# Kernel tuning notes

Measured on AMD Instinct MI355X. Metric: run time of the kernel, lower is better.

Reference implementation:

```python
import jax, jax.numpy as jnp
import numpy as np

SCALE_FACTORS = (0.5, 1.0)
ITERATIONS = (2, 2)
TAU = (1.0, 1.0)
SIGMA = (1.0, 1.0)
SIGMA_CUTOFF = 3.0
EPS = 1e-9
DHW = ('NCDHW', 'OIDHW', 'NCDHW')


def gaussian_kernel1d(sigma):
    radius = int(round(sigma * SIGMA_CUTOFF))
    x = np.arange(-radius, radius + 1, dtype=np.float32)
    k = np.exp(-0.5 * (x / sigma) ** 2)
    return jnp.asarray(k / k.sum())


def smooth3d(vf, kernel):
    # separable depthwise Gaussian over the 3 spatial axes; vf: (B,C,D,H,W)
    C = vf.shape[1]
    n = kernel.shape[0]
    for axis in range(3):
        shape = [1, 1, 1]
        shape[axis] = n
        kern = jnp.broadcast_to(kernel.reshape(1, 1, *shape), (C, 1, *shape))
        vf = jax.lax.conv_general_dilated(vf, kern, (1, 1, 1), 'SAME',
                                          feature_group_count=C, dimension_numbers=DHW)
    return vf


def resize_tri(x, spatial):
    return jax.image.resize(x, x.shape[:2] + tuple(spatial), method='trilinear')


def warp(img, flow):
    # trilinear grid-sample with voxel-space displacement, border clamping
    B, C, D, H, W = img.shape
    gz, gy, gx = jnp.meshgrid(jnp.arange(D, dtype=img.dtype),
                              jnp.arange(H, dtype=img.dtype),
                              jnp.arange(W, dtype=img.dtype), indexing='ij')
    base = jnp.stack([gz, gy, gx])  # (3,D,H,W)

    def one(im, fl):
        z = jnp.clip(base[0] + fl[0], 0.0, D - 1)
        y = jnp.clip(base[1] + fl[1], 0.0, H - 1)
        x = jnp.clip(base[2] + fl[2], 0.0, W - 1)
        z0 = jnp.floor(z); y0 = jnp.floor(y); x0 = jnp.floor(x)
        wz = z - z0; wy = y - y0; wx = x - x0
        z0i = z0.astype(jnp.int32); y0i = y0.astype(jnp.int32); x0i = x0.astype(jnp.int32)
        z1i = jnp.minimum(z0i + 1, D - 1)
        y1i = jnp.minimum(y0i + 1, H - 1)
        x1i = jnp.minimum(x0i + 1, W - 1)

        def g(zi, yi, xi):
            return im[:, zi, yi, xi]  # (C,D,H,W)

        return (g(z0i, y0i, x0i) * (1 - wz) * (1 - wy) * (1 - wx)
                + g(z0i, y0i, x1i) * (1 - wz) * (1 - wy) * wx
                + g(z0i, y1i, x0i) * (1 - wz) * wy * (1 - wx)
                + g(z0i, y1i, x1i) * (1 - wz) * wy * wx
                + g(z1i, y0i, x0i) * wz * (1 - wy) * (1 - wx)
                + g(z1i, y0i, x1i) * wz * (1 - wy) * wx
                + g(z1i, y1i, x0i) * wz * wy * (1 - wx)
                + g(z1i, y1i, x1i) * wz * wy * wx)

    return jax.vmap(one)(img, flow)


def demon_forces(warped, fixed):
    # 'active' demon forces: gradient of the warped moving image
    diff = warped - fixed                                  # (B,1,D,H,W)
    g = jnp.stack(jnp.gradient(warped[:, 0], axis=(1, 2, 3)), axis=1)  # (B,3,D,H,W)
    denom = jnp.sum(g * g, axis=1, keepdims=True) + diff * diff + EPS
    return diff * g / denom


def conv3(x, w, b=None):
    y = jax.lax.conv_general_dilated(x, w, (1, 1, 1), 'SAME', dimension_numbers=DHW)
    return y if b is None else y + b.reshape(1, -1, 1, 1, 1)


def inorm(x):  # InstanceNorm3d, affine=False, eps=1e-5
    m = x.mean(axis=(2, 3, 4), keepdims=True)
    v = x.var(axis=(2, 3, 4), keepdims=True)
    return (x - m) * jax.lax.rsqrt(v + 1e-5)


def mish(x):
    return x * jnp.tanh(jax.nn.softplus(x))


def updater(x, w1, w2, w3, w4, b4):
    x = mish(inorm(conv3(x, w1)))
    x = mish(inorm(conv3(x, w2)))
    x = mish(inorm(conv3(x, w3)))
    return conv3(x, w4, b4)


def match_vf(vf, spatial):
    old = vf.shape[2:]
    if tuple(old) == tuple(spatial):
        return vf
    vf2 = resize_tri(vf, spatial)
    scale = jnp.array([s1 / s2 for s1, s2 in zip(spatial, old)], dtype=vf.dtype)
    return vf2 * scale.reshape(1, 3, 1, 1, 1)


def registration(image, moving, w1, w2, w3, w4, b4):
    vf = None
    for i, (sf, iters) in enumerate(zip(SCALE_FACTORS, ITERATIONS)):
        spatial = tuple(int(s * sf) for s in image.shape[2:])
        si = resize_tri(image, spatial)
        smov = resize_tri(moving, spatial)
        vf = jnp.zeros((image.shape[0], 3) + spatial, image.dtype) if vf is None else match_vf(vf, spatial)
        kernel = gaussian_kernel1d(SIGMA[i]).astype(image.dtype)
        for _ in range(iters):
            warped = warp(smov, vf)
            forces = demon_forces(warped, si)
            feat = jnp.concatenate([forces, si, warped], axis=1)  # 5 channels
            vf = vf + TAU[i] * updater(feat, w1, w2, w3, w4, b4)
            vf = smooth3d(vf, kernel)
    vf = match_vf(vf, image.shape[2:])
    warped_full = warp(moving, vf)
    return warped_full, vf


def setup_inputs() -> dict:
    key = jax.random.key(0)
    ks = jax.random.split(key, 8)
    D = H = W = 96
    return {
        'image': jax.random.uniform(ks[0], (1, 1, D, H, W), jnp.float32),
        'mask': jnp.ones((1, 1, D, H, W), jnp.float32),
        'moving': jax.random.uniform(ks[1], (1, 1, D, H, W), jnp.float32),
        'spacing': jnp.ones((3,), jnp.float32),
        'w1': jax.random.normal(ks[2], (32, 5, 3, 3, 3), jnp.float32) * 0.05,
        'w2': jax.random.normal(ks[3], (64, 32, 3, 3, 3), jnp.float32) * 0.05,
        'w3': jax.random.normal(ks[4], (32, 64, 3, 3, 3), jnp.float32) * 0.05,
        'w4': jax.random.normal(ks[5], (3, 32, 3, 3, 3), jnp.float32) * 0.05,
        'b4': jnp.zeros((3,), jnp.float32),
    }


def reference(image, mask, moving, spacing, w1, w2, w3, w4, b4):
    # mask only feeds metrics/early-stopping (disabled: early_stopping_fn='none');
    # spacing unused since use_image_spacing=False.
    return registration(image, moving, w1, w2, w3, w4, b4)
```

## Files before the change

kernel.cpp:

```cpp
#include <hip/hip_runtime.h>
#include <hip/hip_bf16.h>


#define DEV __device__ __forceinline__
typedef __hip_bfloat16 bf16;
typedef __attribute__((ext_vector_type(8))) short short8;
typedef __attribute__((ext_vector_type(4))) float f32x4;

DEV float bfu(unsigned int u) {
  union { unsigned int i; float f; } x; x.i = u << 16; return x.f;
}
DEV unsigned short fbf(float f) {
  __hip_bfloat16 h = __float2bfloat16(f);
  return __builtin_bit_cast(unsigned short, h);
}

__global__ void zero_k(float* __restrict__ p, int n) {
  int i = blockIdx.x * 256 + threadIdx.x;
  if (i < n) p[i] = 0.f;
}
__global__ void copy_k(const float* __restrict__ in, float* __restrict__ out, int n) {
  int i = blockIdx.x * 256 + threadIdx.x;
  if (i < n) out[i] = in[i];
}

__global__ void pack_wf_k(const float* __restrict__ w, bf16* __restrict__ dst,
                          int NWT, int KB, int COR, int CIR) {
  int idx = blockIdx.x * 256 + threadIdx.x;
  int tot = 27 * NWT * KB * 512;
  if (idx >= tot) return;
  int j = idx & 7;
  int lane = (idx >> 3) & 63;
  int frag = idx >> 9;
  int kb = frag % KB;
  int r2 = frag / KB;
  int nwt = r2 % NWT;
  int off = r2 / NWT;
  int lid = lane & 15, kg = lane >> 4;
  int co = nwt * 16 + lid;
  int ci = (kb * 4 + kg) * 8 + j;
  float v = (co < COR && ci < CIR) ? w[((size_t)co * CIR + ci) * 27 + off] : 0.f;
  dst[idx] = __float2bfloat16(v);
}

DEV int ds_taps(int i, int n_out, int* j0, float* w) {
  if (i == 0) { *j0 = 0; w[0] = 3.f/7.f; w[1] = 3.f/7.f; w[2] = 1.f/7.f; return 3; }
  if (i == n_out - 1) { *j0 = 2*i - 1; w[0] = 1.f/7.f; w[1] = 3.f/7.f; w[2] = 3.f/7.f; return 3; }
  *j0 = 2*i - 1; w[0] = 0.125f; w[1] = 0.375f; w[2] = 0.375f; w[3] = 0.125f; return 4;
}
DEV void up_taps(int i, int n_in, int* j0, int* j1, float* w0, float* w1) {
  if (i & 1) {
    int k = i >> 1;
    if (k + 1 >= n_in) { *j0 = n_in - 1; *j1 = n_in - 1; *w0 = 1.f; *w1 = 0.f; }
    else { *j0 = k; *j1 = k + 1; *w0 = 0.75f; *w1 = 0.25f; }
  } else {
    int k = i >> 1;
    if (k == 0) { *j0 = 0; *j1 = 0; *w0 = 1.f; *w1 = 0.f; }
    else { *j0 = k - 1; *j1 = k; *w0 = 0.25f; *w1 = 0.75f; }
  }
}

__global__ void down2x_k(const float* __restrict__ in, float* __restrict__ out,
                         int Do, int Ho, int Wo) {
  const int Hi = 2 * Ho, Wi = 2 * Wo;
  const int No = Do * Ho * Wo;
  int i = blockIdx.x * 256 + threadIdx.x;
  if (i >= No) return;
  int xo = i % Wo; int t = i / Wo; int yo = t % Ho; int zo = t / Ho;
  int jz0, jy0, jx0; float wz[4], wy[4], wx[4];
  int cz = ds_taps(zo, Do, &jz0, wz);
  int cy = ds_taps(yo, Ho, &jy0, wy);
  int cx = ds_taps(xo, Wo, &jx0, wx);
  float s = 0.f;
  for (int a = 0; a < cz; ++a) {
    const float* pz = in + (size_t)(jz0 + a) * Hi * Wi;
    for (int b = 0; b < cy; ++b) {
      const float* py = pz + (size_t)(jy0 + b) * Wi;
      float wab = wz[a] * wy[b];
      for (int d = 0; d < cx; ++d) s += wab * wx[d] * py[jx0 + d];
    }
  }
  out[i] = s;
}

__global__ void up2x_vf_k(const float* __restrict__ in, float* __restrict__ out,
                          int Do, int Ho, int Wo) {
  const int Di = Do / 2, Hi = Ho / 2, Wi = Wo / 2;
  const int No = Do * Ho * Wo;
  const int c = blockIdx.y;
  int i = blockIdx.x * 256 + threadIdx.x;
  if (i >= No) return;
  int xo = i % Wo; int t = i / Wo; int yo = t % Ho; int zo = t / Ho;
  int jz0, jz1, jy0, jy1, jx0, jx1; float wz0, wz1, wy0, wy1, wx0, wx1;
  up_taps(zo, Di, &jz0, &jz1, &wz0, &wz1);
  up_taps(yo, Hi, &jy0, &jy1, &wy0, &wy1);
  up_taps(xo, Wi, &jx0, &jx1, &wx0, &wx1);
  const float* p = in + (size_t)c * Di * Hi * Wi;
  float v00 = wx0 * p[(jz0 * Hi + jy0) * Wi + jx0] + wx1 * p[(jz0 * Hi + jy0) * Wi + jx1];
  float v01 = wx0 * p[(jz0 * Hi + jy1) * Wi + jx0] + wx1 * p[(jz0 * Hi + jy1) * Wi + jx1];
  float v10 = wx0 * p[(jz1 * Hi + jy0) * Wi + jx0] + wx1 * p[(jz1 * Hi + jy0) * Wi + jx1];
  float v11 = wx0 * p[(jz1 * Hi + jy1) * Wi + jx0] + wx1 * p[(jz1 * Hi + jy1) * Wi + jx1];
  float s = wz0 * (wy0 * v00 + wy1 * v01) + wz1 * (wy0 * v10 + wy1 * v11);
  out[(size_t)c * No + i] = 2.f * s;
}

__global__ void warp_k(const float* __restrict__ img, const float* __restrict__ vf,
                       float* __restrict__ out, int D, int H, int W) {
  const int N = D * H * W;
  int i = blockIdx.x * 256 + threadIdx.x;
  if (i >= N) return;
  int x = i % W; int t = i / W; int y = t % H; int z = t / H;
  float zc = fminf(fmaxf((float)z + vf[i], 0.f), (float)(D - 1));
  float yc = fminf(fmaxf((float)y + vf[(size_t)N + i], 0.f), (float)(H - 1));
  float xc = fminf(fmaxf((float)x + vf[2 * (size_t)N + i], 0.f), (float)(W - 1));
  float zf = floorf(zc), yf = floorf(yc), xf = floorf(xc);
  int z0 = (int)zf, y0 = (int)yf, x0 = (int)xf;
  float wz = zc - zf, wy = yc - yf, wx = xc - xf;
  int z1 = min(z0 + 1, D - 1), y1 = min(y0 + 1, H - 1), x1 = min(x0 + 1, W - 1);
  const int HW = H * W;
  float v000 = img[z0 * HW + y0 * W + x0];
  float v001 = img[z0 * HW + y0 * W + x1];
  float v010 = img[z0 * HW + y1 * W + x0];
  float v011 = img[z0 * HW + y1 * W + x1];
  float v100 = img[z1 * HW + y0 * W + x0];
  float v101 = img[z1 * HW + y0 * W + x1];
  float v110 = img[z1 * HW + y1 * W + x0];
  float v111 = img[z1 * HW + y1 * W + x1];
  float r = v000 * (1 - wz) * (1 - wy) * (1 - wx)
          + v001 * (1 - wz) * (1 - wy) * wx
          + v010 * (1 - wz) * wy * (1 - wx)
          + v011 * (1 - wz) * wy * wx
          + v100 * wz * (1 - wy) * (1 - wx)
          + v101 * wz * (1 - wy) * wx
          + v110 * wz * wy * (1 - wx)
          + v111 * wz * wy * wx;
  out[i] = r;
}

__global__ void forces8_k(const float* __restrict__ wpd, const float* __restrict__ si,
                          bf16* __restrict__ feat, int D, int H, int W) {
  const int N = D * H * W;
  int i = blockIdx.x * 256 + threadIdx.x;
  if (i >= N) return;
  int x = i % W; int t = i / W; int y = t % H; int z = t / H;
  float wv = wpd[i];
  const int HW = H * W;
  float gz = (z == 0) ? (wpd[i + HW] - wv) : (z == D - 1) ? (wv - wpd[i - HW]) : 0.5f * (wpd[i + HW] - wpd[i - HW]);
  float gy = (y == 0) ? (wpd[i + W] - wv) : (y == H - 1) ? (wv - wpd[i - W]) : 0.5f * (wpd[i + W] - wpd[i - W]);
  float gx = (x == 0) ? (wpd[i + 1] - wv) : (x == W - 1) ? (wv - wpd[i - 1]) : 0.5f * (wpd[i + 1] - wpd[i - 1]);
  float s = si[i];
  float diff = wv - s;
  float denom = gz * gz + gy * gy + gx * gx + diff * diff + 1e-9f;
  short8 o;
  o[0] = (short)fbf((diff * gz) / denom);
  o[1] = (short)fbf((diff * gy) / denom);
  o[2] = (short)fbf((diff * gx) / denom);
  o[3] = (short)fbf(s);
  o[4] = (short)fbf(wv);
  o[5] = 0; o[6] = 0; o[7] = 0;
  *(short8*)((short*)feat + (size_t)i * 8) = o;
}

template <int CIN, int COUT, int TZ, int TY, int INS, int REDUCE>
__global__ void __launch_bounds__(512) convmf_k(
    const bf16* __restrict__ act, const bf16* __restrict__ wpk,
    bf16* __restrict__ out, double* __restrict__ pbuf, int D, int H, int W) {
  constexpr int CH = CIN / 8;
  constexpr int HZ = TZ + 2, HY = TY + 2;
  constexpr int HALO = HZ * HY * 18;
  constexpr int MS = TZ * TY / 4;
  constexpr int NS = COUT / 32;
  constexpr int NWT = COUT / 16;
  constexpr int KB = CIN / 32;
  __shared__ short lds[HALO * CIN];
  __shared__ float2 red[8][NS][16];
  const int t = threadIdx.x;
  const int gx0 = blockIdx.x * 16, gy0 = blockIdx.y * TY, gz0 = blockIdx.z * TZ;
  const short* actS = (const short*)act;
  for (int cid = t; cid < HALO * CH; cid += 512) {
    int pos = cid / CH, c = cid - pos * CH;
    int hx = pos % 18; int r = pos / 18; int hy = r % HY; int hz = r / HY;
    int gz = gz0 + hz - 1, gy = gy0 + hy - 1, gx = gx0 + hx - 1;
    uint4 v = {0u, 0u, 0u, 0u};
    if (((unsigned)gz < (unsigned)D) & ((unsigned)gy < (unsigned)H) & ((unsigned)gx < (unsigned)W)) {
      size_t vox = (size_t)(gz * H + gy) * W + gx;
      if (INS == 8) { if (c == 0) v = *(const uint4*)(actS + vox * 8); }
      else v = *(const uint4*)(actS + vox * CIN + c * 8);
    }
    *(uint4*)(lds + pos * CIN + ((c ^ (pos & (CH - 1))) * 8)) = v;
  }
  __syncthreads();
  const int lane = t & 63, wid = t >> 6;
  const int mw = wid & 3, nw = wid >> 2;
  const int lid = lane & 15, kg = lane >> 4;
  f32x4 acc[MS][NS];
#pragma unroll
  for (int ms = 0; ms < MS; ++ms)
#pragma unroll
    for (int n = 0; n < NS; ++n) acc[ms][n] = {0.f, 0.f, 0.f, 0.f};
  int rowpos[MS];
#pragma unroll
  for (int ms = 0; ms < MS; ++ms) {
    int r = mw * MS + ms;
    rowpos[ms] = ((r / TY) * HY + (r % TY)) * 18 + lid;
  }
  const short* wp = (const short*)wpk;
#pragma unroll 1
  for (int kz = 0; kz < 3; ++kz)
#pragma unroll 1
    for (int ky = 0; ky < 3; ++ky) {
      const int delta0 = (kz * HY + ky) * 18;
#pragma unroll
      for (int kx = 0; kx < 3; ++kx) {
        const int off = (kz * 3 + ky) * 3 + kx;
        short8 bq[NS][KB];
#pragma unroll
        for (int n = 0; n < NS; ++n)
#pragma unroll
          for (int kb = 0; kb < KB; ++kb)
            bq[n][kb] = *(const short8*)(wp + ((((size_t)off * NWT + nw * NS + n) * KB + kb) << 9) + lane * 8);
#pragma unroll
        for (int ms = 0; ms < MS; ++ms) {
          int pos = rowpos[ms] + delta0 + kx;
          int sw = pos & (CH - 1);
#pragma unroll
          for (int kb = 0; kb < KB; ++kb) {
            short8 a = *(const short8*)(lds + pos * CIN + (((kb * 4 + kg) ^ sw) * 8));
#pragma unroll
            for (int n = 0; n < NS; ++n)
              acc[ms][n] = __builtin_amdgcn_mfma_f32_16x16x32_bf16(a, bq[n][kb], acc[ms][n], 0, 0, 0);
          }
        }
      }
    }
  const int xe = kg * 4;
#pragma unroll
  for (int ms = 0; ms < MS; ++ms) {
    int r = mw * MS + ms;
    int z = gz0 + r / TY, y = gy0 + r % TY;
    size_t voxb = (size_t)(z * H + y) * W + gx0;
#pragma unroll
    for (int n = 0; n < NS; ++n) {
      int co = nw * NS * 16 + n * 16 + lid;
#pragma unroll
      for (int rg = 0; rg < 4; ++rg)
        out[(voxb + xe + rg) * COUT + co] = __float2bfloat16(acc[ms][n][rg]);
    }
  }
  if (REDUCE) {
#pragma unroll
    for (int n = 0; n < NS; ++n) {
      float s = 0.f, q = 0.f;
#pragma unroll
      for (int ms = 0; ms < MS; ++ms)
#pragma unroll
        for (int rg = 0; rg < 4; ++rg) {
          float v = acc[ms][n][rg];
          s += v; q += v * v;
        }
      s += __shfl_xor(s, 16); q += __shfl_xor(q, 16);
      s += __shfl_xor(s, 32); q += __shfl_xor(q, 32);
      if (lane < 16) red[wid][n][lane] = make_float2(s, q);
    }
    __syncthreads();
    if (t < COUT) {
      const int nw_ = t / (NS * 16);
      const int rem = t - nw_ * NS * 16;
      const int n_ = rem >> 4, lid_ = rem & 15;
      float S = 0.f, Q = 0.f;
#pragma unroll
      for (int m = 0; m < 4; ++m) {
        float2 v = red[nw_ * 4 + m][n_][lid_];
        S += v.x; Q += v.y;
      }
      const int G = gridDim.x * gridDim.y * gridDim.z;
      const int bid = blockIdx.x + gridDim.x * (blockIdx.y + gridDim.y * blockIdx.z);
      pbuf[((size_t)t * G + bid) * 2 + 0] = (double)S;
      pbuf[((size_t)t * G + bid) * 2 + 1] = (double)Q;
    }
  }
}

template <int TZ, int TY>
__global__ void __launch_bounds__(512) conv4mf_k(
    const bf16* __restrict__ act, const bf16* __restrict__ wpk,
    const float* __restrict__ bias, float* __restrict__ vf, int D, int H, int W) {
  constexpr int CH = 4;
  constexpr int HZ = TZ + 2, HY = TY + 2;
  constexpr int HALO = HZ * HY * 18;
  constexpr int MS = TZ * TY / 8;
  __shared__ short lds[HALO * 32];
  const int t = threadIdx.x;
  const int gx0 = blockIdx.x * 16, gy0 = blockIdx.y * TY, gz0 = blockIdx.z * TZ;
  const int N = D * H * W;
  const short* actS = (const short*)act;
  for (int cid = t; cid < HALO * CH; cid += 512) {
    int pos = cid / CH, c = cid - pos * CH;
    int hx = pos % 18; int r = pos / 18; int hy = r % HY; int hz = r / HY;
    int gz = gz0 + hz - 1, gy = gy0 + hy - 1, gx = gx0 + hx - 1;
    uint4 v = {0u, 0u, 0u, 0u};
    if (((unsigned)gz < (unsigned)D) & ((unsigned)gy < (unsigned)H) & ((unsigned)gx < (unsigned)W))
      v = *(const uint4*)(actS + ((size_t)(gz * H + gy) * W + gx) * 32 + c * 8);
    *(uint4*)(lds + pos * 32 + ((c ^ (pos & 3)) * 8)) = v;
  }
  __syncthreads();
  const int lane = t & 63, wid = t >> 6;
  const int lid = lane & 15, kg = lane >> 4;
  f32x4 acc[MS];
#pragma unroll
  for (int ms = 0; ms < MS; ++ms) acc[ms] = {0.f, 0.f, 0.f, 0.f};
  int rowpos[MS];
#pragma unroll
  for (int ms = 0; ms < MS; ++ms) {
    int r = wid * MS + ms;
    rowpos[ms] = ((r / TY) * HY + (r % TY)) * 18 + lid;
  }
  const short* wp = (const short*)wpk;
#pragma unroll 1
  for (int kz = 0; kz < 3; ++kz)
#pragma unroll 1
    for (int ky = 0; ky < 3; ++ky) {
      const int delta0 = (kz * HY + ky) * 18;
#pragma unroll
      for (int kx = 0; kx < 3; ++kx) {
        const int off = (kz * 3 + ky) * 3 + kx;
        short8 b = *(const short8*)(wp + ((size_t)off << 9) + lane * 8);
#pragma unroll
        for (int ms = 0; ms < MS; ++ms) {
          int pos = rowpos[ms] + delta0 + kx;
          int sw = pos & 3;
          short8 a = *(const short8*)(lds + pos * 32 + ((kg ^ sw) * 8));
          acc[ms] = __builtin_amdgcn_mfma_f32_16x16x32_bf16(a, b, acc[ms], 0, 0, 0);
        }
      }
    }
  if (lid < 3) {
    float bs = bias[lid];
#pragma unroll
    for (int ms = 0; ms < MS; ++ms) {
      int r = wid * MS + ms;
      int z = gz0 + r / TY, y = gy0 + r % TY;
      size_t voxb = (size_t)(z * H + y) * W + gx0 + kg * 4;
      float* p = vf + (size_t)lid * N + voxb;
#pragma unroll
      for (int rg = 0; rg < 4; ++rg) p[rg] += acc[ms][rg] + bs;
    }
  }
}

__global__ void stage2_k(const double* __restrict__ pbuf, float2* __restrict__ musc,
                         int N, int G) {
  const int c = blockIdx.x;
  double S = 0, Q = 0;
  for (int g = threadIdx.x; g < G; g += 256) {
    S += pbuf[((size_t)c * G + g) * 2 + 0];
    Q += pbuf[((size_t)c * G + g) * 2 + 1];
  }
  for (int off = 32; off > 0; off >>= 1) {
    S += __shfl_down(S, off); Q += __shfl_down(Q, off);
  }
  __shared__ double ls[4], lq[4];
  const int wid = threadIdx.x >> 6, lane = threadIdx.x & 63;
  if (lane == 0) { ls[wid] = S; lq[wid] = Q; }
  __syncthreads();
  if (threadIdx.x == 0) {
    double St = ls[0] + ls[1] + ls[2] + ls[3];
    double Qt = lq[0] + lq[1] + lq[2] + lq[3];
    double m = St / N;
    double var = Qt / N - m * m;
    musc[c] = make_float2((float)m, (float)(1.0 / sqrt(var + 1e-5)));
  }
}

DEV float mishf(float v) {
  if (v > 20.f) return v;
  float u = __expf(v);
  float w = u * (u + 2.f);
  return v * (w / (w + 2.f));
}

template <int C>
__global__ void inorm_vc_k(bf16* __restrict__ x, const float2* __restrict__ musc, int N) {
  constexpr int CP = C / 2;
  constexpr int VPB = 256 / CP;
  const int cp = threadIdx.x & (CP - 1);
  const int vt = threadIdx.x / CP;
  float2 m0 = musc[2 * cp], m1 = musc[2 * cp + 1];
  unsigned int* p = (unsigned int*)x;
  int v0 = blockIdx.x * (4 * VPB) + vt;
#pragma unroll
  for (int r = 0; r < 4; ++r) {
    int v = v0 + r * VPB;
    size_t idx = (size_t)v * CP + cp;
    unsigned int u = p[idx];
    float a = mishf((bfu(u & 0xffffu) - m0.x) * m0.y);
    float b = mishf((bfu(u >> 16) - m1.x) * m1.y);
    p[idx] = (unsigned int)fbf(a) | ((unsigned int)fbf(b) << 16);
  }
}

template <int AXIS>
__global__ void smooth_k(const float* __restrict__ in, float* __restrict__ out,
                         int D, int H, int W) {
  const int N = D * H * W;
  const int c = blockIdx.y;
  int i = blockIdx.x * 256 + threadIdx.x;
  if (i >= N) return;
  int x = i % W; int t = i / W; int y = t % H; int z = t / H;
  const int coord = AXIS == 0 ? z : AXIS == 1 ? y : x;
  const int len = AXIS == 0 ? D : AXIS == 1 ? H : W;
  const int stride = AXIS == 0 ? H * W : AXIS == 1 ? W : 1;
  const float k1 = 0.60653065971263342f, k2 = 0.13533528323661270f, k3 = 0.011108996538242306f;
  const float kn = 1.f / (1.f + 2.f * (k1 + k2 + k3));
  const float gw[4] = {kn, k1 * kn, k2 * kn, k3 * kn};
  const float* p = in + (size_t)c * N;
  float s = gw[0] * p[i];
#pragma unroll
  for (int tt = 1; tt <= 3; ++tt) {
    if (coord - tt >= 0) s += gw[tt] * p[i - tt * stride];
    if (coord + tt < len) s += gw[tt] * p[i + tt * stride];
  }
  out[(size_t)c * N + i] = s;
}

extern "C" void kernel_launch(void* const* d_in, const int* in_sizes, int n_in,
                              void* d_out, int out_size, void* d_ws, size_t ws_size,
                              hipStream_t stream) {
  const float* image  = (const float*)d_in[0];
  const float* moving = (const float*)d_in[2];
  const float* w1 = (const float*)d_in[4];
  const float* w2 = (const float*)d_in[5];
  const float* w3 = (const float*)d_in[6];
  const float* w4 = (const float*)d_in[7];
  const float* b4 = (const float*)d_in[8];
  float* out = (float*)d_out;

  const int D1 = 96; const int N1 = D1 * D1 * D1;
  const int D0 = 48; const int N0 = D0 * D0 * D0;

  char* wsp = (char*)d_ws;
  double* pbuf  = (double*)wsp;          wsp += (size_t)64 * 13824 * 2 * 8;
  float2* musc  = (float2*)wsp;          wsp += 1024;
  bf16* w1p     = (bf16*)wsp;            wsp += 27 * 2 * 1 * 512 * 2;
  bf16* w2p     = (bf16*)wsp;            wsp += 27 * 4 * 1 * 512 * 2;
  bf16* w3p     = (bf16*)wsp;            wsp += 27 * 2 * 2 * 512 * 2;
  bf16* w4p     = (bf16*)wsp;            wsp += 27 * 1 * 1 * 512 * 2;
  float* si0    = (float*)wsp;           wsp += (size_t)N0 * 4;
  float* smov0  = (float*)wsp;           wsp += (size_t)N0 * 4;
  float* vf0    = (float*)wsp;           wsp += 3 * (size_t)N1 * 4;
  float* vf1    = (float*)wsp;           wsp += 3 * (size_t)N1 * 4;
  float* warped = (float*)wsp;           wsp += (size_t)N1 * 4;
  bf16* feat    = (bf16*)wsp;            wsp += 8 * (size_t)N1 * 2;
  bf16* bufA    = (bf16*)wsp;            wsp += 32 * (size_t)N1 * 2;
  bf16* bufB    = (bf16*)wsp;            wsp += 64 * (size_t)N1 * 2;

  pack_wf_k<<<(27 * 2 * 512 + 255) / 256, 256, 0, stream>>>(w1, w1p, 2, 1, 32, 5);
  pack_wf_k<<<(27 * 4 * 512 + 255) / 256, 256, 0, stream>>>(w2, w2p, 4, 1, 64, 32);
  pack_wf_k<<<(27 * 4 * 512 + 255) / 256, 256, 0, stream>>>(w3, w3p, 2, 2, 32, 64);
  pack_wf_k<<<(27 * 1 * 512 + 255) / 256, 256, 0, stream>>>(w4, w4p, 1, 1, 3, 32);

  down2x_k<<<N0 / 256, 256, 0, stream>>>(image, si0, D0, D0, D0);
  down2x_k<<<N0 / 256, 256, 0, stream>>>(moving, smov0, D0, D0, D0);
  zero_k<<<3 * N0 / 256, 256, 0, stream>>>(vf0, 3 * N0);

  float* vfc = vf0;
  float* vfa = vf1;

  auto run_level = [&](const float* si, const float* smov, int Dd) {
    const int N = Dd * Dd * Dd;
    const int nb = N / 256;
    const dim3 g1(Dd / 16, Dd / 4, Dd / 4);
    const dim3 g3(Dd / 16, Dd / 4, Dd / 2);
    const int G1 = g1.x * g1.y * g1.z;
    const int G3 = g3.x * g3.y * g3.z;
    for (int it = 0; it < 2; ++it) {
      warp_k<<<nb, 256, 0, stream>>>(smov, vfc, warped, Dd, Dd, Dd);
      forces8_k<<<nb, 256, 0, stream>>>(warped, si, feat, Dd, Dd, Dd);

      convmf_k<32, 32, 4, 4, 8, 1><<<g1, 512, 0, stream>>>(feat, w1p, bufA, pbuf, Dd, Dd, Dd);
      stage2_k<<<32, 256, 0, stream>>>(pbuf, musc, N, G1);
      inorm_vc_k<32><<<N / 64, 256, 0, stream>>>(bufA, musc, N);

      convmf_k<32, 64, 4, 4, 32, 1><<<g1, 512, 0, stream>>>(bufA, w2p, bufB, pbuf, Dd, Dd, Dd);
      stage2_k<<<64, 256, 0, stream>>>(pbuf, musc, N, G1);
      inorm_vc_k<64><<<N / 32, 256, 0, stream>>>(bufB, musc, N);

      convmf_k<64, 32, 2, 4, 64, 1><<<g3, 512, 0, stream>>>(bufB, w3p, bufA, pbuf, Dd, Dd, Dd);
      stage2_k<<<32, 256, 0, stream>>>(pbuf, musc, N, G3);
      inorm_vc_k<32><<<N / 64, 256, 0, stream>>>(bufA, musc, N);

      conv4mf_k<4, 4><<<g1, 512, 0, stream>>>(bufA, w4p, b4, vfc, Dd, Dd, Dd);

      smooth_k<0><<<dim3(nb, 3), 256, 0, stream>>>(vfc, vfa, Dd, Dd, Dd);
      smooth_k<1><<<dim3(nb, 3), 256, 0, stream>>>(vfa, vfc, Dd, Dd, Dd);
      smooth_k<2><<<dim3(nb, 3), 256, 0, stream>>>(vfc, vfa, Dd, Dd, Dd);
      { float* tmp = vfc; vfc = vfa; vfa = tmp; }
    }
  };

  run_level(si0, smov0, D0);

  up2x_vf_k<<<dim3(N1 / 256, 3), 256, 0, stream>>>(vfc, vfa, D1, D1, D1);
  { float* tmp = vfc; vfc = vfa; vfa = tmp; }

  run_level(image, moving, D1);

  warp_k<<<N1 / 256, 256, 0, stream>>>(moving, vfc, out, D1, D1, D1);
  copy_k<<<3 * N1 / 256, 256, 0, stream>>>(vfc, out + N1, 3 * N1);
}
```

Baseline: 1.353 ms.

## Use smaller 2x4 spatial tiles with one row per wave in MFMA convs

```diff
diff --git a/kernel.cpp b/kernel.cpp
--- a/kernel.cpp
+++ b/kernel.cpp
@@ -161,16 +161,15 @@
   *(short8*)((short*)feat + (size_t)i * 8) = o;
 }
 
-template <int CIN, int COUT, int TZ, int TY, int INS, int REDUCE>
+template <int CIN, int COUT, int INS, int REDUCE>
 __global__ void __launch_bounds__(512) convmf_k(
     const bf16* __restrict__ act, const bf16* __restrict__ wpk,
     bf16* __restrict__ out, double* __restrict__ pbuf, int D, int H, int W) {
+  constexpr int TZ = 2, TY = 4;
   constexpr int CH = CIN / 8;
   constexpr int HZ = TZ + 2, HY = TY + 2;
   constexpr int HALO = HZ * HY * 18;
-  constexpr int MS = TZ * TY / 4;
-  constexpr int NS = COUT / 32;
-  constexpr int NWT = COUT / 16;
+  constexpr int NS = COUT / 16;
   constexpr int KB = CIN / 32;
   __shared__ short lds[HALO * CIN];
   __shared__ float2 red[8][NS][16];
@@ -191,19 +190,11 @@
   }
   __syncthreads();
   const int lane = t & 63, wid = t >> 6;
-  const int mw = wid & 3, nw = wid >> 2;
   const int lid = lane & 15, kg = lane >> 4;
-  f32x4 acc[MS][NS];
-#pragma unroll
-  for (int ms = 0; ms < MS; ++ms)
-#pragma unroll
-    for (int n = 0; n < NS; ++n) acc[ms][n] = {0.f, 0.f, 0.f, 0.f};
-  int rowpos[MS];
-#pragma unroll
-  for (int ms = 0; ms < MS; ++ms) {
-    int r = mw * MS + ms;
-    rowpos[ms] = ((r / TY) * HY + (r % TY)) * 18 + lid;
-  }
+  f32x4 acc[NS];
+#pragma unroll
+  for (int n = 0; n < NS; ++n) acc[n] = {0.f, 0.f, 0.f, 0.f};
+  const int rowpos = ((wid / TY) * HY + (wid % TY)) * 18 + lid;
   const short* wp = (const short*)wpk;
 #pragma unroll 1
   for (int kz = 0; kz < 3; ++kz)
@@ -218,33 +209,28 @@
         for (int n = 0; n < NS; ++n)
 #pragma unroll
           for (int kb = 0; kb < KB; ++kb)
-            bq[n][kb] = *(const short8*)(wp + ((((size_t)off * NWT + nw * NS + n) * KB + kb) << 9) + lane * 8);
-#pragma unroll
-        for (int ms = 0; ms < MS; ++ms) {
-          int pos = rowpos[ms] + delta0 + kx;
-          int sw = pos & (CH - 1);
-#pragma unroll
-          for (int kb = 0; kb < KB; ++kb) {
-            short8 a = *(const short8*)(lds + pos * CIN + (((kb * 4 + kg) ^ sw) * 8));
-#pragma unroll
-            for (int n = 0; n < NS; ++n)
-              acc[ms][n] = __builtin_amdgcn_mfma_f32_16x16x32_bf16(a, bq[n][kb], acc[ms][n], 0, 0, 0);
-          }
+            bq[n][kb] = *(const short8*)(wp + ((((size_t)off * NS + n) * KB + kb) << 9) + lane * 8);
+        const int pos = rowpos + delta0 + kx;
+        const int sw = pos & (CH - 1);
+#pragma unroll
+        for (int kb = 0; kb < KB; ++kb) {
+          short8 a = *(const short8*)(lds + pos * CIN + (((kb * 4 + kg) ^ sw) * 8));
+#pragma unroll
+          for (int n = 0; n < NS; ++n)
+            acc[n] = __builtin_amdgcn_mfma_f32_16x16x32_bf16(a, bq[n][kb], acc[n], 0, 0, 0);
         }
       }
     }
   const int xe = kg * 4;
-#pragma unroll
-  for (int ms = 0; ms < MS; ++ms) {
-    int r = mw * MS + ms;
-    int z = gz0 + r / TY, y = gy0 + r % TY;
+  {
+    int z = gz0 + wid / TY, y = gy0 + wid % TY;
     size_t voxb = (size_t)(z * H + y) * W + gx0;
 #pragma unroll
     for (int n = 0; n < NS; ++n) {
-      int co = nw * NS * 16 + n * 16 + lid;
+      int co = n * 16 + lid;
 #pragma unroll
       for (int rg = 0; rg < 4; ++rg)
-        out[(voxb + xe + rg) * COUT + co] = __float2bfloat16(acc[ms][n][rg]);
+        out[(voxb + xe + rg) * COUT + co] = __float2bfloat16(acc[n][rg]);
     }
   }
   if (REDUCE) {
@@ -252,25 +238,21 @@
     for (int n = 0; n < NS; ++n) {
       float s = 0.f, q = 0.f;
 #pragma unroll
-      for (int ms = 0; ms < MS; ++ms)
-#pragma unroll
-        for (int rg = 0; rg < 4; ++rg) {
-          float v = acc[ms][n][rg];
-          s += v; q += v * v;
-        }
+      for (int rg = 0; rg < 4; ++rg) {
+        float v = acc[n][rg];
+        s += v; q += v * v;
+      }
       s += __shfl_xor(s, 16); q += __shfl_xor(q, 16);
       s += __shfl_xor(s, 32); q += __shfl_xor(q, 32);
       if (lane < 16) red[wid][n][lane] = make_float2(s, q);
     }
     __syncthreads();
     if (t < COUT) {
-      const int nw_ = t / (NS * 16);
-      const int rem = t - nw_ * NS * 16;
-      const int n_ = rem >> 4, lid_ = rem & 15;
+      const int n_ = t >> 4, lid_ = t & 15;
       float S = 0.f, Q = 0.f;
 #pragma unroll
-      for (int m = 0; m < 4; ++m) {
-        float2 v = red[nw_ * 4 + m][n_][lid_];
+      for (int m = 0; m < 8; ++m) {
+        float2 v = red[m][n_][lid_];
         S += v.x; Q += v.y;
       }
       const int G = gridDim.x * gridDim.y * gridDim.z;
@@ -281,14 +263,13 @@
   }
 }
 
-template <int TZ, int TY>
 __global__ void __launch_bounds__(512) conv4mf_k(
     const bf16* __restrict__ act, const bf16* __restrict__ wpk,
     const float* __restrict__ bias, float* __restrict__ vf, int D, int H, int W) {
+  constexpr int TZ = 2, TY = 4;
   constexpr int CH = 4;
   constexpr int HZ = TZ + 2, HY = TY + 2;
   constexpr int HALO = HZ * HY * 18;
-  constexpr int MS = TZ * TY / 8;
   __shared__ short lds[HALO * 32];
   const int t = threadIdx.x;
   const int gx0 = blockIdx.x * 16, gy0 = blockIdx.y * TY, gz0 = blockIdx.z * TZ;
@@ -306,15 +287,8 @@
   __syncthreads();
   const int lane = t & 63, wid = t >> 6;
   const int lid = lane & 15, kg = lane >> 4;
-  f32x4 acc[MS];
-#pragma unroll
-  for (int ms = 0; ms < MS; ++ms) acc[ms] = {0.f, 0.f, 0.f, 0.f};
-  int rowpos[MS];
-#pragma unroll
-  for (int ms = 0; ms < MS; ++ms) {
-    int r = wid * MS + ms;
-    rowpos[ms] = ((r / TY) * HY + (r % TY)) * 18 + lid;
-  }
+  f32x4 acc = {0.f, 0.f, 0.f, 0.f};
+  const int rowpos = ((wid / TY) * HY + (wid % TY)) * 18 + lid;
   const short* wp = (const short*)wpk;
 #pragma unroll 1
   for (int kz = 0; kz < 3; ++kz)
@@ -325,26 +299,19 @@
       for (int kx = 0; kx < 3; ++kx) {
         const int off = (kz * 3 + ky) * 3 + kx;
         short8 b = *(const short8*)(wp + ((size_t)off << 9) + lane * 8);
-#pragma unroll
-        for (int ms = 0; ms < MS; ++ms) {
-          int pos = rowpos[ms] + delta0 + kx;
-          int sw = pos & 3;
-          short8 a = *(const short8*)(lds + pos * 32 + ((kg ^ sw) * 8));
-          acc[ms] = __builtin_amdgcn_mfma_f32_16x16x32_bf16(a, b, acc[ms], 0, 0, 0);
-        }
+        const int pos = rowpos + delta0 + kx;
+        const int sw = pos & 3;
+        short8 a = *(const short8*)(lds + pos * 32 + ((kg ^ sw) * 8));
+        acc = __builtin_amdgcn_mfma_f32_16x16x32_bf16(a, b, acc, 0, 0, 0);
       }
     }
   if (lid < 3) {
     float bs = bias[lid];
-#pragma unroll
-    for (int ms = 0; ms < MS; ++ms) {
-      int r = wid * MS + ms;
-      int z = gz0 + r / TY, y = gy0 + r % TY;
-      size_t voxb = (size_t)(z * H + y) * W + gx0 + kg * 4;
-      float* p = vf + (size_t)lid * N + voxb;
-#pragma unroll
-      for (int rg = 0; rg < 4; ++rg) p[rg] += acc[ms][rg] + bs;
-    }
+    int z = gz0 + wid / TY, y = gy0 + wid % TY;
+    size_t voxb = (size_t)(z * H + y) * W + gx0 + kg * 4;
+    float* p = vf + (size_t)lid * N + voxb;
+#pragma unroll
+    for (int rg = 0; rg < 4; ++rg) p[rg] += acc[rg] + bs;
   }
 }
 
@@ -469,27 +436,25 @@
   auto run_level = [&](const float* si, const float* smov, int Dd) {
     const int N = Dd * Dd * Dd;
     const int nb = N / 256;
-    const dim3 g1(Dd / 16, Dd / 4, Dd / 4);
-    const dim3 g3(Dd / 16, Dd / 4, Dd / 2);
-    const int G1 = g1.x * g1.y * g1.z;
-    const int G3 = g3.x * g3.y * g3.z;
+    const dim3 gc(Dd / 16, Dd / 4, Dd / 2);
+    const int G = gc.x * gc.y * gc.z;
     for (int it = 0; it < 2; ++it) {
       warp_k<<<nb, 256, 0, stream>>>(smov, vfc, warped, Dd, Dd, Dd);
       forces8_k<<<nb, 256, 0, stream>>>(warped, si, feat, Dd, Dd, Dd);
 
-      convmf_k<32, 32, 4, 4, 8, 1><<<g1, 512, 0, stream>>>(feat, w1p, bufA, pbuf, Dd, Dd, Dd);
-      stage2_k<<<32, 256, 0, stream>>>(pbuf, musc, N, G1);
+      convmf_k<32, 32, 8, 1><<<gc, 512, 0, stream>>>(feat, w1p, bufA, pbuf, Dd, Dd, Dd);
+      stage2_k<<<32, 256, 0, stream>>>(pbuf, musc, N, G);
       inorm_vc_k<32><<<N / 64, 256, 0, stream>>>(bufA, musc, N);
 
-      convmf_k<32, 64, 4, 4, 32, 1><<<g1, 512, 0, stream>>>(bufA, w2p, bufB, pbuf, Dd, Dd, Dd);
-      stage2_k<<<64, 256, 0, stream>>>(pbuf, musc, N, G1);
+      convmf_k<32, 64, 32, 1><<<gc, 512, 0, stream>>>(bufA, w2p, bufB, pbuf, Dd, Dd, Dd);
+      stage2_k<<<64, 256, 0, stream>>>(pbuf, musc, N, G);
       inorm_vc_k<64><<<N / 32, 256, 0, stream>>>(bufB, musc, N);
 
-      convmf_k<64, 32, 2, 4, 64, 1><<<g3, 512, 0, stream>>>(bufB, w3p, bufA, pbuf, Dd, Dd, Dd);
-      stage2_k<<<32, 256, 0, stream>>>(pbuf, musc, N, G3);
+      convmf_k<64, 32, 64, 1><<<gc, 512, 0, stream>>>(bufB, w3p, bufA, pbuf, Dd, Dd, Dd);
+      stage2_k<<<32, 256, 0, stream>>>(pbuf, musc, N, G);
       inorm_vc_k<32><<<N / 64, 256, 0, stream>>>(bufA, musc, N);
 
-      conv4mf_k<4, 4><<<g1, 512, 0, stream>>>(bufA, w4p, b4, vfc, Dd, Dd, Dd);
+      conv4mf_k<<<gc, 512, 0, stream>>>(bufA, w4p, b4, vfc, Dd, Dd, Dd);
 
       smooth_k<0><<<dim3(nb, 3), 256, 0, stream>>>(vfc, vfa, Dd, Dd, Dd);
       smooth_k<1><<<dim3(nb, 3), 256, 0, stream>>>(vfa, vfc, Dd, Dd, Dd);
```

Result: slower. 1.813 ms (+34.0%).

## Switch conv kernels to 32x32x16 MFMA tiles and shrink conv1 channel padding

Applied to the files above, without the earlier changes.

```diff
diff --git a/kernel.cpp b/kernel.cpp
--- a/kernel.cpp
+++ b/kernel.cpp
@@ -6,6 +6,7 @@
 typedef __hip_bfloat16 bf16;
 typedef __attribute__((ext_vector_type(8))) short short8;
 typedef __attribute__((ext_vector_type(4))) float f32x4;
+typedef __attribute__((ext_vector_type(16))) float f32x16;
 
 DEV float bfu(unsigned int u) {
   union { unsigned int i; float f; } x; x.i = u << 16; return x.f;
@@ -36,9 +37,26 @@
   int r2 = frag / KB;
   int nwt = r2 % NWT;
   int off = r2 / NWT;
-  int lid = lane & 15, kg = lane >> 4;
-  int co = nwt * 16 + lid;
-  int ci = (kb * 4 + kg) * 8 + j;
+  int co = nwt * 16 + (lane & 15);
+  int ci = (kb * 4 + (lane >> 4)) * 8 + j;
+  float v = (co < COR && ci < CIR) ? w[((size_t)co * CIR + ci) * 27 + off] : 0.f;
+  dst[idx] = __float2bfloat16(v);
+}
+
+__global__ void pack_w32_k(const float* __restrict__ w, bf16* __restrict__ dst,
+                           int NT, int KB, int COR, int CIR) {
+  int idx = blockIdx.x * 256 + threadIdx.x;
+  int tot = 27 * NT * KB * 512;
+  if (idx >= tot) return;
+  int j = idx & 7;
+  int lane = (idx >> 3) & 63;
+  int frag = idx >> 9;
+  int kb = frag % KB;
+  int r2 = frag / KB;
+  int n = r2 % NT;
+  int off = r2 / NT;
+  int co = n * 32 + (lane & 31);
+  int ci = kb * 16 + (lane >> 5) * 8 + j;
   float v = (co < COR && ci < CIR) ? w[((size_t)co * CIR + ci) * 27 + off] : 0.f;
   dst[idx] = __float2bfloat16(v);
 }
@@ -161,23 +179,23 @@
   *(short8*)((short*)feat + (size_t)i * 8) = o;
 }
 
-template <int CIN, int COUT, int TZ, int TY, int INS, int REDUCE>
-__global__ void __launch_bounds__(512) convmf_k(
+template <int CIN, int COUT, int INS, int REDUCE, int TZ, int TY>
+__global__ void __launch_bounds__(TZ* TY * 32) convmf32_k(
     const bf16* __restrict__ act, const bf16* __restrict__ wpk,
     bf16* __restrict__ out, double* __restrict__ pbuf, int D, int H, int W) {
+  constexpr int WAVES = TZ * TY / 2;
+  constexpr int THREADS = WAVES * 64;
   constexpr int CH = CIN / 8;
   constexpr int HZ = TZ + 2, HY = TY + 2;
   constexpr int HALO = HZ * HY * 18;
-  constexpr int MS = TZ * TY / 4;
-  constexpr int NS = COUT / 32;
-  constexpr int NWT = COUT / 16;
-  constexpr int KB = CIN / 32;
+  constexpr int NT = COUT / 32;
+  constexpr int KB = CIN / 16;
   __shared__ short lds[HALO * CIN];
-  __shared__ float2 red[8][NS][16];
+  __shared__ float2 red[WAVES][NT][32];
   const int t = threadIdx.x;
   const int gx0 = blockIdx.x * 16, gy0 = blockIdx.y * TY, gz0 = blockIdx.z * TZ;
   const short* actS = (const short*)act;
-  for (int cid = t; cid < HALO * CH; cid += 512) {
+  for (int cid = t; cid < HALO * CH; cid += THREADS) {
     int pos = cid / CH, c = cid - pos * CH;
     int hx = pos % 18; int r = pos / 18; int hy = r % HY; int hz = r / HY;
     int gz = gz0 + hz - 1, gy = gy0 + hy - 1, gx = gx0 + hx - 1;
@@ -191,19 +209,15 @@
   }
   __syncthreads();
   const int lane = t & 63, wid = t >> 6;
-  const int mw = wid & 3, nw = wid >> 2;
-  const int lid = lane & 15, kg = lane >> 4;
-  f32x4 acc[MS][NS];
-#pragma unroll
-  for (int ms = 0; ms < MS; ++ms)
-#pragma unroll
-    for (int n = 0; n < NS; ++n) acc[ms][n] = {0.f, 0.f, 0.f, 0.f};
-  int rowpos[MS];
-#pragma unroll
-  for (int ms = 0; ms < MS; ++ms) {
-    int r = mw * MS + ms;
-    rowpos[ms] = ((r / TY) * HY + (r % TY)) * 18 + lid;
-  }
+  const int m = lane & 31;
+  const int g2 = lane >> 5;
+  f32x16 acc[NT];
+#pragma unroll
+  for (int n = 0; n < NT; ++n)
+#pragma unroll
+    for (int r16 = 0; r16 < 16; ++r16) acc[n][r16] = 0.f;
+  const int r = 2 * wid + (m >> 4);
+  const int rowpos = ((r / TY) * HY + (r % TY)) * 18 + (m & 15);
   const short* wp = (const short*)wpk;
 #pragma unroll 1
   for (int kz = 0; kz < 3; ++kz)
@@ -213,64 +227,52 @@
 #pragma unroll
       for (int kx = 0; kx < 3; ++kx) {
         const int off = (kz * 3 + ky) * 3 + kx;
-        short8 bq[NS][KB];
-#pragma unroll
-        for (int n = 0; n < NS; ++n)
+        short8 bq[NT][KB];
+#pragma unroll
+        for (int n = 0; n < NT; ++n)
 #pragma unroll
           for (int kb = 0; kb < KB; ++kb)
-            bq[n][kb] = *(const short8*)(wp + ((((size_t)off * NWT + nw * NS + n) * KB + kb) << 9) + lane * 8);
-#pragma unroll
-        for (int ms = 0; ms < MS; ++ms) {
-          int pos = rowpos[ms] + delta0 + kx;
-          int sw = pos & (CH - 1);
-#pragma unroll
-          for (int kb = 0; kb < KB; ++kb) {
-            short8 a = *(const short8*)(lds + pos * CIN + (((kb * 4 + kg) ^ sw) * 8));
-#pragma unroll
-            for (int n = 0; n < NS; ++n)
-              acc[ms][n] = __builtin_amdgcn_mfma_f32_16x16x32_bf16(a, bq[n][kb], acc[ms][n], 0, 0, 0);
-          }
+            bq[n][kb] = *(const short8*)(wp + ((((size_t)off * NT + n) * KB + kb) << 9) + lane * 8);
+        const int pos = rowpos + delta0 + kx;
+        const int sw = pos & (CH - 1);
+#pragma unroll
+        for (int kb = 0; kb < KB; ++kb) {
+          short8 a = *(const short8*)(lds + pos * CIN + (((kb * 2 + g2) ^ sw) * 8));
+#pragma unroll
+          for (int n = 0; n < NT; ++n)
+            acc[n] = __builtin_amdgcn_mfma_f32_32x32x16_bf16(a, bq[n][kb], acc[n], 0, 0, 0);
         }
       }
     }
-  const int xe = kg * 4;
-#pragma unroll
-  for (int ms = 0; ms < MS; ++ms) {
-    int r = mw * MS + ms;
-    int z = gz0 + r / TY, y = gy0 + r % TY;
-    size_t voxb = (size_t)(z * H + y) * W + gx0;
-#pragma unroll
-    for (int n = 0; n < NS; ++n) {
-      int co = nw * NS * 16 + n * 16 + lid;
-#pragma unroll
-      for (int rg = 0; rg < 4; ++rg)
-        out[(voxb + xe + rg) * COUT + co] = __float2bfloat16(acc[ms][n][rg]);
-    }
+#pragma unroll
+  for (int reg = 0; reg < 16; ++reg) {
+    const int mm = (reg & 3) + 8 * (reg >> 2) + 4 * g2;
+    const int rr = 2 * wid + (mm >> 4);
+    const int z = gz0 + rr / TY, y = gy0 + rr % TY;
+    const size_t vox = (size_t)(z * H + y) * W + gx0 + (mm & 15);
+#pragma unroll
+    for (int n = 0; n < NT; ++n)
+      out[vox * COUT + n * 32 + (lane & 31)] = __float2bfloat16(acc[n][reg]);
   }
   if (REDUCE) {
 #pragma unroll
-    for (int n = 0; n < NS; ++n) {
+    for (int n = 0; n < NT; ++n) {
       float s = 0.f, q = 0.f;
 #pragma unroll
-      for (int ms = 0; ms < MS; ++ms)
-#pragma unroll
-        for (int rg = 0; rg < 4; ++rg) {
-          float v = acc[ms][n][rg];
-          s += v; q += v * v;
-        }
-      s += __shfl_xor(s, 16); q += __shfl_xor(q, 16);
+      for (int r16 = 0; r16 < 16; ++r16) {
+        float v = acc[n][r16];
+        s += v; q += v * v;
+      }
       s += __shfl_xor(s, 32); q += __shfl_xor(q, 32);
-      if (lane < 16) red[wid][n][lane] = make_float2(s, q);
+      if (lane < 32) red[wid][n][lane] = make_float2(s, q);
     }
     __syncthreads();
     if (t < COUT) {
-      const int nw_ = t / (NS * 16);
-      const int rem = t - nw_ * NS * 16;
-      const int n_ = rem >> 4, lid_ = rem & 15;
+      const int n_ = t >> 5, co = t & 31;
       float S = 0.f, Q = 0.f;
 #pragma unroll
-      for (int m = 0; m < 4; ++m) {
-        float2 v = red[nw_ * 4 + m][n_][lid_];
+      for (int mw = 0; mw < WAVES; ++mw) {
+        float2 v = red[mw][n_][co];
         S += v.x; Q += v.y;
       }
       const int G = gridDim.x * gridDim.y * gridDim.z;
@@ -441,9 +443,9 @@
   char* wsp = (char*)d_ws;
   double* pbuf  = (double*)wsp;          wsp += (size_t)64 * 13824 * 2 * 8;
   float2* musc  = (float2*)wsp;          wsp += 1024;
-  bf16* w1p     = (bf16*)wsp;            wsp += 27 * 2 * 1 * 512 * 2;
-  bf16* w2p     = (bf16*)wsp;            wsp += 27 * 4 * 1 * 512 * 2;
-  bf16* w3p     = (bf16*)wsp;            wsp += 27 * 2 * 2 * 512 * 2;
+  bf16* w1p     = (bf16*)wsp;            wsp += 27 * 1 * 1 * 512 * 2;
+  bf16* w2p     = (bf16*)wsp;            wsp += 27 * 2 * 2 * 512 * 2;
+  bf16* w3p     = (bf16*)wsp;            wsp += 27 * 1 * 4 * 512 * 2;
   bf16* w4p     = (bf16*)wsp;            wsp += 27 * 1 * 1 * 512 * 2;
   float* si0    = (float*)wsp;           wsp += (size_t)N0 * 4;
   float* smov0  = (float*)wsp;           wsp += (size_t)N0 * 4;
@@ -454,9 +456,9 @@
   bf16* bufA    = (bf16*)wsp;            wsp += 32 * (size_t)N1 * 2;
   bf16* bufB    = (bf16*)wsp;            wsp += 64 * (size_t)N1 * 2;
 
-  pack_wf_k<<<(27 * 2 * 512 + 255) / 256, 256, 0, stream>>>(w1, w1p, 2, 1, 32, 5);
-  pack_wf_k<<<(27 * 4 * 512 + 255) / 256, 256, 0, stream>>>(w2, w2p, 4, 1, 64, 32);
-  pack_wf_k<<<(27 * 4 * 512 + 255) / 256, 256, 0, stream>>>(w3, w3p, 2, 2, 32, 64);
+  pack_w32_k<<<(27 * 1 * 512 + 255) / 256, 256, 0, stream>>>(w1, w1p, 1, 1, 32, 5);
+  pack_w32_k<<<(27 * 4 * 512 + 255) / 256, 256, 0, stream>>>(w2, w2p, 2, 2, 64, 32);
+  pack_w32_k<<<(27 * 4 * 512 + 255) / 256, 256, 0, stream>>>(w3, w3p, 1, 4, 32, 64);
   pack_wf_k<<<(27 * 1 * 512 + 255) / 256, 256, 0, stream>>>(w4, w4p, 1, 1, 3, 32);
 
   down2x_k<<<N0 / 256, 256, 0, stream>>>(image, si0, D0, D0, D0);
@@ -477,15 +479,15 @@
       warp_k<<<nb, 256, 0, stream>>>(smov, vfc, warped, Dd, Dd, Dd);
       forces8_k<<<nb, 256, 0, stream>>>(warped, si, feat, Dd, Dd, Dd);
 
-      convmf_k<32, 32, 4, 4, 8, 1><<<g1, 512, 0, stream>>>(feat, w1p, bufA, pbuf, Dd, Dd, Dd);
+      convmf32_k<16, 32, 8, 1, 4, 4><<<g1, 512, 0, stream>>>(feat, w1p, bufA, pbuf, Dd, Dd, Dd);
       stage2_k<<<32, 256, 0, stream>>>(pbuf, musc, N, G1);
       inorm_vc_k<32><<<N / 64, 256, 0, stream>>>(bufA, musc, N);
 
-      convmf_k<32, 64, 4, 4, 32, 1><<<g1, 512, 0, stream>>>(bufA, w2p, bufB, pbuf, Dd, Dd, Dd);
+      convmf32_k<32, 64, 32, 1, 4, 4><<<g1, 512, 0, stream>>>(bufA, w2p, bufB, pbuf, Dd, Dd, Dd);
       stage2_k<<<64, 256, 0, stream>>>(pbuf, musc, N, G1);
       inorm_vc_k<64><<<N / 32, 256, 0, stream>>>(bufB, musc, N);
 
-      convmf_k<64, 32, 2, 4, 64, 1><<<g3, 512, 0, stream>>>(bufB, w3p, bufA, pbuf, Dd, Dd, Dd);
+      convmf32_k<64, 32, 64, 1, 2, 4><<<g3, 256, 0, stream>>>(bufB, w3p, bufA, pbuf, Dd, Dd, Dd);
       stage2_k<<<32, 256, 0, stream>>>(pbuf, musc, N, G3);
       inorm_vc_k<32><<<N / 64, 256, 0, stream>>>(bufA, musc, N);
 
```

After: 1.491 ms. 10.2% more time.
